# Kernel optimization log

Measured on AMD Instinct MI355X. Metric: run time of the kernel, lower is better.

The kernel has to match this reference:

```python
import jax, jax.numpy as jnp
import numpy as np
from jax import lax

CLIP = 5.0
LN_EPS = 1e-5


def _embed(feats, mean, std, W, b, g, beta):
    # InputNorm (eval mode, count>1): normalize with running stats, clamp.
    h = jnp.clip((feats - mean) / std, -CLIP, CLIP)
    h = lax.stop_gradient(h)  # torch runs InputNorm under no_grad
    # Linear + ReLU
    h = jax.nn.relu(h @ W + b)
    # LayerNorm over d_model
    mu = h.mean(-1, keepdims=True)
    var = ((h - mu) ** 2).mean(-1, keepdims=True)
    return (h - mu) / jnp.sqrt(var + LN_EPS) * g + beta


def setup_inputs() -> dict:
    key = jax.random.key(0)
    ks = jax.random.split(key, 8)
    nA, fA = 300000, 32
    nB, fB = 150000, 48
    d = 256
    B = 512
    inp = {
        "featsA": jax.random.normal(ks[0], (nA, fA), jnp.float32),
        "featsB": jax.random.normal(ks[1], (nB, fB), jnp.float32),
        "normA_mean": jnp.zeros((fA,), jnp.float32),
        "normA_std": jnp.ones((fA,), jnp.float32),
        "normB_mean": jnp.zeros((fB,), jnp.float32),
        "normB_std": jnp.ones((fB,), jnp.float32),
        "WA": jax.random.normal(ks[2], (fA, d), jnp.float32) / np.sqrt(fA),
        "bA": jnp.zeros((d,), jnp.float32),
        "lnA_g": jnp.ones((d,), jnp.float32),
        "lnA_b": jnp.zeros((d,), jnp.float32),
        "WB_": jax.random.normal(ks[3], (fB, d), jnp.float32) / np.sqrt(fB),
        "bB": jnp.zeros((d,), jnp.float32),
        "lnB_g": jnp.ones((d,), jnp.float32),
        "lnB_b": jnp.zeros((d,), jnp.float32),
        "Wback": jax.random.normal(ks[4], (d, d), jnp.float32) / np.sqrt(d),
        "bback": jnp.zeros((d,), jnp.float32),
        "Wv": jax.random.normal(ks[5], (d, 1), jnp.float32) / np.sqrt(d),
        "bv": jnp.zeros((1,), jnp.float32),
        "batch_index": jax.random.randint(ks[6], (nA + nB,), 0, B, jnp.int64)
        if jax.config.jax_enable_x64 else jax.random.randint(ks[6], (nA + nB,), 0, B, jnp.int32).astype(jnp.int32),
        "num_obs": B,
    }
    return inp


def reference(featsA, featsB, normA_mean, normA_std, normB_mean, normB_std,
              WA, bA, lnA_g, lnA_b, WB_, bB, lnB_g, lnB_b,
              Wback, bback, Wv, bv, batch_index, num_obs):
    # Per-entity-type embedding stacks, concatenated in entity-type order
    xA = _embed(featsA, normA_mean, normA_std, WA, bA, lnA_g, lnA_b)
    xB = _embed(featsB, normB_mean, normB_std, WB_, bB, lnB_g, lnB_b)
    x = jnp.concatenate([xA, xB], axis=0)          # [N, d]
    x = jax.nn.relu(x @ Wback + bback)              # backbone
    # torch_scatter mean pooling over observations
    sums = jax.ops.segment_sum(x, batch_index, num_segments=num_obs)
    counts = jax.ops.segment_sum(jnp.ones((x.shape[0],), x.dtype), batch_index,
                                 num_segments=num_obs)
    pooled = sums / jnp.maximum(counts, 1.0)[:, None]  # empty segments -> 0
    return pooled @ Wv + bv                          # [num_obs, 1]
```

## Files before the change

kernel.cpp:

```cpp
#include <hip/hip_runtime.h>

#define NSEG 512
#define NSPLIT 32

typedef __attribute__((ext_vector_type(8))) short short8;
typedef __attribute__((ext_vector_type(4))) short short4v;
typedef __attribute__((ext_vector_type(4))) float floatx4;

#define WS_WAT   0
#define WS_WBT2  16384
#define WS_W2GA  49152
#define WS_W2GB  180224
#define WS_C1A   311296
#define WS_C2A   312320
#define WS_C1B   313344
#define WS_C2B   314368
#define WS_INVA  315392
#define WS_INVB  315520
#define WS_VPART 315712
#define WS_CPART 381248
#define WS_NF    446848

__device__ __forceinline__ short f2bf(float f) {
  unsigned u = __builtin_bit_cast(unsigned, f);
  u += 0x7FFFu + ((u >> 16) & 1u);
  return (short)(u >> 16);
}

__global__ void prep_kernel(const float* __restrict__ WA, const float* __restrict__ WB,
                            const float* __restrict__ Wback,
                            const float* __restrict__ gA, const float* __restrict__ betaA,
                            const float* __restrict__ gB, const float* __restrict__ betaB,
                            const float* __restrict__ bback,
                            const float* __restrict__ sA, const float* __restrict__ sB,
                            char* __restrict__ ws) {
  short* waT  = (short*)(ws + WS_WAT);
  short* wbT2 = (short*)(ws + WS_WBT2);
  short* w2gA = (short*)(ws + WS_W2GA);
  short* w2gB = (short*)(ws + WS_W2GB);
  float* c1A = (float*)(ws + WS_C1A);
  float* c2A = (float*)(ws + WS_C2A);
  float* c1B = (float*)(ws + WS_C1B);
  float* c2B = (float*)(ws + WS_C2B);
  float* invA = (float*)(ws + WS_INVA);
  float* invB = (float*)(ws + WS_INVB);
  float* vz   = (float*)(ws + WS_VPART);
  int tid = blockIdx.x * blockDim.x + threadIdx.x;
  int stride = gridDim.x * blockDim.x;
  if (tid < 32) invA[tid] = 1.0f / sA[tid];
  if (tid < 48) invB[tid] = 1.0f / sB[tid];
  for (int i = tid; i < 32*256; i += stride) {
    int n = i >> 5, k = i & 31;
    waT[i] = f2bf(WA[k*256 + n]);
  }
  for (int i = tid; i < 256*64; i += stride) {
    int n = i >> 6, k = i & 63;
    wbT2[i] = (k < 48) ? f2bf(WB[k*256 + n]) : (short)0;
  }
  for (int i = tid; i < 256*256; i += stride) {
    int n = i >> 8, k = i & 255;
    float w = Wback[k*256 + n];
    w2gA[i] = f2bf(gA[k] * w);
    w2gB[i] = f2bf(gB[k] * w);
  }
  if (blockIdx.x < 4 && threadIdx.x < 256) {
    int n = threadIdx.x;
    int which = blockIdx.x;
    const float* coef = (which == 0) ? gA : (which == 1) ? betaA : (which == 2) ? gB : betaB;
    float a = 0.f;
    #pragma unroll 8
    for (int k = 0; k < 256; k++) a = fmaf(coef[k], Wback[k*256 + n], a);
    if (which == 0)      c1A[n] = a;
    else if (which == 1) c2A[n] = a + bback[n];
    else if (which == 2) c1B[n] = a;
    else                 c2B[n] = a + bback[n];
  }
  for (int i = tid; i < 2*NSPLIT*NSEG; i += stride) vz[i] = 0.0f;
}

__global__ __launch_bounds__(256) void norm_kernel(
    const float* __restrict__ fA, const float* __restrict__ fB,
    const float* __restrict__ mA, const float* __restrict__ mB,
    const char* __restrict__ ws, short* __restrict__ nfA, short* __restrict__ nfB,
    int rowsApad, int nA, int rowsBpad, int nB)
{
  const float* invA = (const float*)(ws + WS_INVA);
  const float* invB = (const float*)(ws + WS_INVB);
  int tid = blockIdx.x * blockDim.x + threadIdx.x;
  int stride = gridDim.x * blockDim.x;
  int chunksA = rowsApad * 4;
  int chunksB = rowsBpad * 8;
  for (int i = tid; i < chunksA + chunksB; i += stride) {
    short8 o = {0,0,0,0,0,0,0,0};
    if (i < chunksA) {
      int row = i >> 2, c0 = (i & 3) * 8;
      if (row < nA) {
        const float* fp = fA + (size_t)row*32 + c0;
        floatx4 x0 = *(const floatx4*)fp;
        floatx4 x1 = *(const floatx4*)(fp + 4);
        floatx4 mv0 = *(const floatx4*)(mA + c0);
        floatx4 mv1 = *(const floatx4*)(mA + c0 + 4);
        floatx4 iv0 = *(const floatx4*)(invA + c0);
        floatx4 iv1 = *(const floatx4*)(invA + c0 + 4);
        #pragma unroll
        for (int e = 0; e < 4; e++) {
          float h0 = fminf(fmaxf((x0[e] - mv0[e]) * iv0[e], -5.0f), 5.0f);
          float h1 = fminf(fmaxf((x1[e] - mv1[e]) * iv1[e], -5.0f), 5.0f);
          o[e] = f2bf(h0);  o[4+e] = f2bf(h1);
        }
      }
      *(short8*)(nfA + (size_t)row*32 + c0) = o;
    } else {
      int j = i - chunksA;
      int row = j >> 3, c0 = (j & 7) * 8;
      if (row < nB && c0 < 48) {
        const float* fp = fB + (size_t)row*48 + c0;
        floatx4 x0 = *(const floatx4*)fp;
        floatx4 x1 = *(const floatx4*)(fp + 4);
        floatx4 mv0 = *(const floatx4*)(mB + c0);
        floatx4 mv1 = *(const floatx4*)(mB + c0 + 4);
        floatx4 iv0 = *(const floatx4*)(invB + c0);
        floatx4 iv1 = *(const floatx4*)(invB + c0 + 4);
        #pragma unroll
        for (int e = 0; e < 4; e++) {
          float h0 = fminf(fmaxf((x0[e] - mv0[e]) * iv0[e], -5.0f), 5.0f);
          float h1 = fminf(fmaxf((x1[e] - mv1[e]) * iv1[e], -5.0f), 5.0f);
          o[e] = f2bf(h0);  o[4+e] = f2bf(h1);
        }
      }
      *(short8*)(nfB + (size_t)row*64 + c0) = o;
    }
  }
}

template <bool PRE>
__global__ __launch_bounds__(256, 4) void fused_kernel(
    const float* __restrict__ featsA, const float* __restrict__ featsB,
    const short* __restrict__ nfA, const short* __restrict__ nfB,
    const float* __restrict__ mA, const float* __restrict__ mB,
    const float* __restrict__ bA, const float* __restrict__ bB,
    const float* __restrict__ Wv, const int* __restrict__ bidx,
    const char* __restrict__ ws, float* __restrict__ vpart, float* __restrict__ cpart,
    int tilesA, int nA, int nB)
{
  __shared__ __attribute__((aligned(16))) short ztile[64*264];
  __shared__ __attribute__((aligned(16))) float sred[64][4];
  __shared__ __attribute__((aligned(16))) float s2red[64][4];
  __shared__ __attribute__((aligned(16))) float vpw[64][4];

  const int tid  = threadIdx.x;
  const int wave = tid >> 6;
  const int lane = tid & 63;
  const int l15  = lane & 15;
  const int quad = lane >> 4;

  const bool isA = (blockIdx.x < (unsigned)tilesA);
  const int  tb  = isA ? blockIdx.x : (blockIdx.x - tilesA);
  const int  r0  = tb * 64;
  const int  nrows = isA ? nA : nB;
  const int  valid = min(64, nrows - r0);
  const float* feats = isA ? featsA : featsB;
  const short* nf    = isA ? nfA : nfB;
  const float* meanp = isA ? mA : mB;
  const float* invp  = (const float*)(ws + (isA ? WS_INVA : WS_INVB));
  const float* biasp = isA ? bA : bB;
  const short* weT   = (const short*)(ws + (isA ? WS_WAT : WS_WBT2));
  const short* w2gT  = (const short*)(ws + (isA ? WS_W2GA : WS_W2GB));
  const float* c1p   = (const float*)(ws + (isA ? WS_C1A : WS_C1B));
  const float* c2p   = (const float*)(ws + (isA ? WS_C2A : WS_C2B));
  const int f       = isA ? 32 : 48;
  const int kstride = isA ? 32 : 64;
  const int ksteps  = isA ? 1 : 2;

  floatx4 acc1[4][4];
  #pragma unroll
  for (int mt = 0; mt < 4; mt++)
    #pragma unroll
    for (int nt = 0; nt < 4; nt++)
      acc1[mt][nt] = 0.0f;

  for (int kk = 0; kk < ksteps; kk++) {
    short8 bfw[4];
    #pragma unroll
    for (int nt = 0; nt < 4; nt++)
      bfw[nt] = *(const short8*)(weT + (size_t)(64*wave + 16*nt + l15) * kstride + kk*32 + quad*8);

    if (PRE) {
      #pragma unroll
      for (int mt = 0; mt < 4; mt++) {
        short8 a = *(const short8*)(nf + (size_t)(r0 + 16*mt + l15) * kstride + kk*32 + quad*8);
        #pragma unroll
        for (int nt = 0; nt < 4; nt++)
          acc1[mt][nt] = __builtin_amdgcn_mfma_f32_16x16x32_bf16(bfw[nt], a, acc1[mt][nt], 0, 0, 0);
      }
    } else {
      const int k0 = kk*32 + quad*8;
      const bool kvalid = (k0 < f);
      floatx4 mv0 = {0,0,0,0}, mv1 = {0,0,0,0}, iv0 = {1,1,1,1}, iv1 = {1,1,1,1};
      if (kvalid) {
        mv0 = *(const floatx4*)(meanp + k0);  mv1 = *(const floatx4*)(meanp + k0 + 4);
        iv0 = *(const floatx4*)(invp + k0);   iv1 = *(const floatx4*)(invp + k0 + 4);
      }
      #pragma unroll
      for (int mt = 0; mt < 4; mt++) {
        short8 a = {0,0,0,0,0,0,0,0};
        int row = 16*mt + l15;
        if (kvalid && row < valid) {
          const float* fp = feats + (size_t)(r0 + row) * f + k0;
          floatx4 x0 = *(const floatx4*)fp;
          floatx4 x1 = *(const floatx4*)(fp + 4);
          #pragma unroll
          for (int e = 0; e < 4; e++) {
            float h0 = (x0[e] - mv0[e]) * iv0[e];
            h0 = fminf(fmaxf(h0, -5.0f), 5.0f);
            a[e] = f2bf(h0);
            float h1 = (x1[e] - mv1[e]) * iv1[e];
            h1 = fminf(fmaxf(h1, -5.0f), 5.0f);
            a[4+e] = f2bf(h1);
          }
        }
        #pragma unroll
        for (int nt = 0; nt < 4; nt++)
          acc1[mt][nt] = __builtin_amdgcn_mfma_f32_16x16x32_bf16(bfw[nt], a, acc1[mt][nt], 0, 0, 0);
      }
    }
  }

  float sacc[4], s2acc[4];
  #pragma unroll
  for (int mt = 0; mt < 4; mt++) { sacc[mt] = 0.f; s2acc[mt] = 0.f; }

  #pragma unroll
  for (int nt = 0; nt < 4; nt++) {
    const int c0 = 64*wave + 16*nt + 4*quad;
    floatx4 b1v = *(const floatx4*)(biasp + c0);
    #pragma unroll
    for (int mt = 0; mt < 4; mt++) {
      short4v pk;
      #pragma unroll
      for (int r = 0; r < 4; r++) {
        float h = fmaxf(acc1[mt][nt][r] + b1v[r], 0.0f);
        sacc[mt] += h;
        s2acc[mt] = fmaf(h, h, s2acc[mt]);
        pk[r] = f2bf(h);
      }
      *(short4v*)(ztile + (16*mt + l15)*264 + c0) = pk;
    }
  }
  #pragma unroll
  for (int mt = 0; mt < 4; mt++) {
    float s = sacc[mt], s2 = s2acc[mt];
    s += __shfl_xor(s, 16, 64);  s2 += __shfl_xor(s2, 16, 64);
    s += __shfl_xor(s, 32, 64);  s2 += __shfl_xor(s2, 32, 64);
    if (lane < 16) {
      sred[16*mt + lane][wave] = s;
      s2red[16*mt + lane][wave] = s2;
    }
  }
  __syncthreads();

  float rsv[4], mrsv[4];
  #pragma unroll
  for (int mt = 0; mt < 4; mt++) {
    int row = 16*mt + l15;
    floatx4 sv  = *(const floatx4*)sred[row];
    floatx4 s2v = *(const floatx4*)s2red[row];
    float s  = sv[0] + sv[1] + sv[2] + sv[3];
    float s2 = s2v[0] + s2v[1] + s2v[2] + s2v[3];
    float mu  = s * (1.0f/256.0f);
    float var = fmaxf(s2 * (1.0f/256.0f) - mu*mu, 0.0f);
    float rs  = rsqrtf(var + 1e-5f);
    rsv[mt]  = rs;
    mrsv[mt] = mu * rs;
  }

  floatx4 acc2[4][4];
  #pragma unroll
  for (int mt = 0; mt < 4; mt++)
    #pragma unroll
    for (int nt = 0; nt < 4; nt++)
      acc2[mt][nt] = 0.0f;

  #pragma unroll 2
  for (int kk = 0; kk < 8; kk++) {
    short8 bf[4];
    #pragma unroll
    for (int nt = 0; nt < 4; nt++)
      bf[nt] = *(const short8*)(w2gT + (size_t)(64*wave + 16*nt + l15)*256 + kk*32 + quad*8);
    #pragma unroll
    for (int mt = 0; mt < 4; mt++) {
      short8 a = *(const short8*)(ztile + (16*mt + l15)*264 + kk*32 + quad*8);
      #pragma unroll
      for (int nt = 0; nt < 4; nt++)
        acc2[mt][nt] = __builtin_amdgcn_mfma_f32_16x16x32_bf16(bf[nt], a, acc2[mt][nt], 0, 0, 0);
    }
  }

  float pv[4] = {0.f, 0.f, 0.f, 0.f};
  #pragma unroll
  for (int nt = 0; nt < 4; nt++) {
    const int c0 = 64*wave + 16*nt + 4*quad;
    floatx4 c1v = *(const floatx4*)(c1p + c0);
    floatx4 c2v = *(const floatx4*)(c2p + c0);
    floatx4 wvv = *(const floatx4*)(Wv + c0);
    #pragma unroll
    for (int mt = 0; mt < 4; mt++) {
      float rs = rsv[mt], mrs = mrsv[mt];
      #pragma unroll
      for (int r = 0; r < 4; r++) {
        float t = fmaf(-mrs, c1v[r], c2v[r]);
        float y = fmaf(rs, acc2[mt][nt][r], t);
        y = fmaxf(y, 0.0f);
        pv[mt] = fmaf(y, wvv[r], pv[mt]);
      }
    }
  }
  #pragma unroll
  for (int mt = 0; mt < 4; mt++) {
    float p = pv[mt];
    p += __shfl_xor(p, 16, 64);
    p += __shfl_xor(p, 32, 64);
    if (lane < 16) vpw[16*mt + lane][wave] = p;
  }
  __syncthreads();

  if (tid < valid) {
    floatx4 vv = *(const floatx4*)vpw[tid];
    float v = vv[0] + vv[1] + vv[2] + vv[3];
    int g = (isA ? r0 : (nA + r0)) + tid;
    int seg = bidx[g];
    int split = blockIdx.x & (NSPLIT - 1);
    atomicAdd(&vpart[split*NSEG + seg], v);
    atomicAdd(&cpart[split*NSEG + seg], 1.0f);
  }
}

__global__ void final_kernel(const float* __restrict__ vpart, const float* __restrict__ cpart,
                             const float* __restrict__ bv, float* __restrict__ out, int nseg) {
  int s = blockIdx.x * blockDim.x + threadIdx.x;
  if (s < nseg) {
    float a = 0.0f, c = 0.0f;
    #pragma unroll 8
    for (int i = 0; i < NSPLIT; i++) { a += vpart[i*NSEG + s]; c += cpart[i*NSEG + s]; }
    out[s] = a / fmaxf(c, 1.0f) + bv[0];
  }
}

extern "C" void kernel_launch(void* const* d_in, const int* in_sizes, int n_in,
                              void* d_out, int out_size, void* d_ws, size_t ws_size,
                              hipStream_t stream) {
  const float* featsA = (const float*)d_in[0];
  const float* featsB = (const float*)d_in[1];
  const float* mA     = (const float*)d_in[2];
  const float* sA     = (const float*)d_in[3];
  const float* mB     = (const float*)d_in[4];
  const float* sB     = (const float*)d_in[5];
  const float* WA     = (const float*)d_in[6];
  const float* bA     = (const float*)d_in[7];
  const float* gA     = (const float*)d_in[8];
  const float* betaA  = (const float*)d_in[9];
  const float* WB     = (const float*)d_in[10];
  const float* bB     = (const float*)d_in[11];
  const float* gB     = (const float*)d_in[12];
  const float* betaB  = (const float*)d_in[13];
  const float* Wback  = (const float*)d_in[14];
  const float* bback  = (const float*)d_in[15];
  const float* Wv     = (const float*)d_in[16];
  const float* bv     = (const float*)d_in[17];
  const int*   bidx   = (const int*)d_in[18];

  const int nA = in_sizes[0] / 32;
  const int nB = in_sizes[1] / 48;
  char* ws = (char*)d_ws;
  float* vpart = (float*)(ws + WS_VPART);
  float* cpart = (float*)(ws + WS_CPART);
  float* out = (float*)d_out;

  const int tilesA = (nA + 63) / 64;
  const int tilesB = (nB + 63) / 64;
  const int rowsApad = tilesA * 64;
  const int rowsBpad = tilesB * 64;
  const size_t nfa_off = WS_NF;
  const size_t nfb_off = nfa_off + (size_t)rowsApad * 32 * 2;
  const size_t ws_need = nfb_off + (size_t)rowsBpad * 64 * 2;
  const bool pre = (ws_size >= ws_need);
  short* nfA = (short*)(ws + nfa_off);
  short* nfB = (short*)(ws + nfb_off);

  prep_kernel<<<256, 256, 0, stream>>>(WA, WB, Wback, gA, betaA, gB, betaB,
                                       bback, sA, sB, ws);

  if (pre) {
    const int chunks = rowsApad * 4 + rowsBpad * 8;
    int nblk = (chunks + 255) / 256;
    if (nblk > 2048) nblk = 2048;
    norm_kernel<<<nblk, 256, 0, stream>>>(featsA, featsB, mA, mB, ws, nfA, nfB,
                                          rowsApad, nA, rowsBpad, nB);
    fused_kernel<true><<<tilesA + tilesB, 256, 0, stream>>>(
        featsA, featsB, nfA, nfB, mA, mB, bA, bB, Wv, bidx, ws, vpart, cpart,
        tilesA, nA, nB);
  } else {
    fused_kernel<false><<<tilesA + tilesB, 256, 0, stream>>>(
        featsA, featsB, nfA, nfB, mA, mB, bA, bB, Wv, bidx, ws, vpart, cpart,
        tilesA, nA, nB);
  }

  if (out_size > 0)
    final_kernel<<<(out_size + 255) / 256, 256, 0, stream>>>(vpart, cpart, bv, out, out_size);
}
```

Measured before the change: 309.0 us.

## Fuse weight prep into normalization kernel and specialize tile body per entity type

Merges the weight-preparation kernel and the feature normalization kernel into one launch, with each block computing the inverse std into shared memory so normalization need not wait for a prior kernel. Adds a templated per-type tile body with compile-time K stride and step count, plus hoisted base pointers for the MFMA loops. The aim is to cut one launch and its serialization gap and to let the compiler unroll and simplify address math in the main fused kernel. When workspace is too small, the fused kernel still reads invA/invB from the workspace, which the merged kernel writes, so that fallback path keeps working.

```diff
diff --git a/kernel.cpp b/kernel.cpp
--- a/kernel.cpp
+++ b/kernel.cpp
@@ -27,67 +27,67 @@
   return (short)(u >> 16);
 }
 
-__global__ void prep_kernel(const float* __restrict__ WA, const float* __restrict__ WB,
-                            const float* __restrict__ Wback,
-                            const float* __restrict__ gA, const float* __restrict__ betaA,
-                            const float* __restrict__ gB, const float* __restrict__ betaB,
-                            const float* __restrict__ bback,
-                            const float* __restrict__ sA, const float* __restrict__ sB,
-                            char* __restrict__ ws) {
-  short* waT  = (short*)(ws + WS_WAT);
-  short* wbT2 = (short*)(ws + WS_WBT2);
-  short* w2gA = (short*)(ws + WS_W2GA);
-  short* w2gB = (short*)(ws + WS_W2GB);
-  float* c1A = (float*)(ws + WS_C1A);
-  float* c2A = (float*)(ws + WS_C2A);
-  float* c1B = (float*)(ws + WS_C1B);
-  float* c2B = (float*)(ws + WS_C2B);
-  float* invA = (float*)(ws + WS_INVA);
-  float* invB = (float*)(ws + WS_INVB);
-  float* vz   = (float*)(ws + WS_VPART);
+__global__ __launch_bounds__(256) void prep_norm_kernel(
+    const float* __restrict__ fA, const float* __restrict__ fB,
+    const float* __restrict__ mA, const float* __restrict__ mB,
+    const float* __restrict__ sA, const float* __restrict__ sB,
+    const float* __restrict__ WA, const float* __restrict__ WB,
+    const float* __restrict__ Wback,
+    const float* __restrict__ gA, const float* __restrict__ betaA,
+    const float* __restrict__ gB, const float* __restrict__ betaB,
+    const float* __restrict__ bback,
+    char* __restrict__ ws, short* __restrict__ nfA, short* __restrict__ nfB,
+    int rowsApad, int nA, int rowsBpad, int nB)
+{
+  __shared__ float sinv[80];
+  if (threadIdx.x < 32) sinv[threadIdx.x] = 1.0f / sA[threadIdx.x];
+  else if (threadIdx.x < 80) sinv[threadIdx.x] = 1.0f / sB[threadIdx.x - 32];
+  __syncthreads();
+  const float* invAl = sinv;
+  const float* invBl = sinv + 32;
+
   int tid = blockIdx.x * blockDim.x + threadIdx.x;
   int stride = gridDim.x * blockDim.x;
-  if (tid < 32) invA[tid] = 1.0f / sA[tid];
-  if (tid < 48) invB[tid] = 1.0f / sB[tid];
-  for (int i = tid; i < 32*256; i += stride) {
-    int n = i >> 5, k = i & 31;
-    waT[i] = f2bf(WA[k*256 + n]);
-  }
-  for (int i = tid; i < 256*64; i += stride) {
-    int n = i >> 6, k = i & 63;
-    wbT2[i] = (k < 48) ? f2bf(WB[k*256 + n]) : (short)0;
-  }
-  for (int i = tid; i < 256*256; i += stride) {
-    int n = i >> 8, k = i & 255;
-    float w = Wback[k*256 + n];
-    w2gA[i] = f2bf(gA[k] * w);
-    w2gB[i] = f2bf(gB[k] * w);
-  }
-  if (blockIdx.x < 4 && threadIdx.x < 256) {
+
+  if (blockIdx.x < 4) {
     int n = threadIdx.x;
     int which = blockIdx.x;
     const float* coef = (which == 0) ? gA : (which == 1) ? betaA : (which == 2) ? gB : betaB;
     float a = 0.f;
     #pragma unroll 8
     for (int k = 0; k < 256; k++) a = fmaf(coef[k], Wback[k*256 + n], a);
-    if (which == 0)      c1A[n] = a;
-    else if (which == 1) c2A[n] = a + bback[n];
-    else if (which == 2) c1B[n] = a;
-    else                 c2B[n] = a + bback[n];
-  }
-  for (int i = tid; i < 2*NSPLIT*NSEG; i += stride) vz[i] = 0.0f;
-}
-
-__global__ __launch_bounds__(256) void norm_kernel(
-    const float* __restrict__ fA, const float* __restrict__ fB,
-    const float* __restrict__ mA, const float* __restrict__ mB,
-    const char* __restrict__ ws, short* __restrict__ nfA, short* __restrict__ nfB,
-    int rowsApad, int nA, int rowsBpad, int nB)
-{
-  const float* invA = (const float*)(ws + WS_INVA);
-  const float* invB = (const float*)(ws + WS_INVB);
-  int tid = blockIdx.x * blockDim.x + threadIdx.x;
-  int stride = gridDim.x * blockDim.x;
+    float* dst = (float*)(ws + ((which == 0) ? WS_C1A : (which == 1) ? WS_C2A
+                               : (which == 2) ? WS_C1B : WS_C2B));
+    dst[n] = a + ((which & 1) ? bback[n] : 0.0f);
+  }
+
+  {
+    short* waT  = (short*)(ws + WS_WAT);
+    short* wbT2 = (short*)(ws + WS_WBT2);
+    short* w2gA = (short*)(ws + WS_W2GA);
+    short* w2gB = (short*)(ws + WS_W2GB);
+    float* invA = (float*)(ws + WS_INVA);
+    float* invB = (float*)(ws + WS_INVB);
+    float* vz   = (float*)(ws + WS_VPART);
+    if (tid < 32) invA[tid] = invAl[tid];
+    if (tid < 48) invB[tid] = invBl[tid];
+    for (int i = tid; i < 32*256; i += stride) {
+      int n = i >> 5, k = i & 31;
+      waT[i] = f2bf(WA[k*256 + n]);
+    }
+    for (int i = tid; i < 256*64; i += stride) {
+      int n = i >> 6, k = i & 63;
+      wbT2[i] = (k < 48) ? f2bf(WB[k*256 + n]) : (short)0;
+    }
+    for (int i = tid; i < 256*256; i += stride) {
+      int n = i >> 8, k = i & 255;
+      float w = Wback[k*256 + n];
+      w2gA[i] = f2bf(gA[k] * w);
+      w2gB[i] = f2bf(gB[k] * w);
+    }
+    for (int i = tid; i < 2*NSPLIT*NSEG; i += stride) vz[i] = 0.0f;
+  }
+
   int chunksA = rowsApad * 4;
   int chunksB = rowsBpad * 8;
   for (int i = tid; i < chunksA + chunksB; i += stride) {
@@ -100,8 +100,8 @@
         floatx4 x1 = *(const floatx4*)(fp + 4);
         floatx4 mv0 = *(const floatx4*)(mA + c0);
         floatx4 mv1 = *(const floatx4*)(mA + c0 + 4);
-        floatx4 iv0 = *(const floatx4*)(invA + c0);
-        floatx4 iv1 = *(const floatx4*)(invA + c0 + 4);
+        floatx4 iv0 = *(const floatx4*)(invAl + c0);
+        floatx4 iv1 = *(const floatx4*)(invAl + c0 + 4);
         #pragma unroll
         for (int e = 0; e < 4; e++) {
           float h0 = fminf(fmaxf((x0[e] - mv0[e]) * iv0[e], -5.0f), 5.0f);
@@ -119,8 +119,8 @@
         floatx4 x1 = *(const floatx4*)(fp + 4);
         floatx4 mv0 = *(const floatx4*)(mB + c0);
         floatx4 mv1 = *(const floatx4*)(mB + c0 + 4);
-        floatx4 iv0 = *(const floatx4*)(invB + c0);
-        floatx4 iv1 = *(const floatx4*)(invB + c0 + 4);
+        floatx4 iv0 = *(const floatx4*)(invBl + c0);
+        floatx4 iv1 = *(const floatx4*)(invBl + c0 + 4);
         #pragma unroll
         for (int e = 0; e < 4; e++) {
           float h0 = fminf(fmaxf((x0[e] - mv0[e]) * iv0[e], -5.0f), 5.0f);
@@ -130,6 +130,158 @@
       }
       *(short8*)(nfB + (size_t)row*64 + c0) = o;
     }
+  }
+}
+
+template <int KSTR, int KSTEPS>
+__device__ __forceinline__ void tile_body(
+    const short* __restrict__ nfb,
+    const short* __restrict__ weT, const short* __restrict__ w2gT,
+    const float* __restrict__ biasp, const float* __restrict__ c1p,
+    const float* __restrict__ c2p, const float* __restrict__ Wv,
+    const int* __restrict__ bidx, float* __restrict__ vpart, float* __restrict__ cpart,
+    short* ztile, float (*sred)[4], float (*s2red)[4], float (*vpw)[4],
+    int valid, int gbase, int split, int tid)
+{
+  const int wave = tid >> 6;
+  const int lane = tid & 63;
+  const int l15  = lane & 15;
+  const int quad = lane >> 4;
+
+  floatx4 acc1[4][4];
+  #pragma unroll
+  for (int mt = 0; mt < 4; mt++)
+    #pragma unroll
+    for (int nt = 0; nt < 4; nt++)
+      acc1[mt][nt] = 0.0f;
+
+  const short* nfp = nfb + l15*KSTR + quad*8;
+  const short* wep = weT + (64*wave + l15)*KSTR + quad*8;
+  #pragma unroll
+  for (int kk = 0; kk < KSTEPS; kk++) {
+    short8 bfw[4];
+    #pragma unroll
+    for (int nt = 0; nt < 4; nt++)
+      bfw[nt] = *(const short8*)(wep + nt*16*KSTR + kk*32);
+    #pragma unroll
+    for (int mt = 0; mt < 4; mt++) {
+      short8 a = *(const short8*)(nfp + mt*16*KSTR + kk*32);
+      #pragma unroll
+      for (int nt = 0; nt < 4; nt++)
+        acc1[mt][nt] = __builtin_amdgcn_mfma_f32_16x16x32_bf16(bfw[nt], a, acc1[mt][nt], 0, 0, 0);
+    }
+  }
+
+  float sacc[4] = {0.f,0.f,0.f,0.f}, s2acc[4] = {0.f,0.f,0.f,0.f};
+  {
+    short* ztw = ztile + l15*264 + 64*wave + 4*quad;
+    const float* bp = biasp + 64*wave + 4*quad;
+    #pragma unroll
+    for (int nt = 0; nt < 4; nt++) {
+      floatx4 b1v = *(const floatx4*)(bp + 16*nt);
+      #pragma unroll
+      for (int mt = 0; mt < 4; mt++) {
+        short4v pk;
+        #pragma unroll
+        for (int r = 0; r < 4; r++) {
+          float h = fmaxf(acc1[mt][nt][r] + b1v[r], 0.0f);
+          sacc[mt] += h;
+          s2acc[mt] = fmaf(h, h, s2acc[mt]);
+          pk[r] = f2bf(h);
+        }
+        *(short4v*)(ztw + mt*16*264 + nt*16) = pk;
+      }
+    }
+  }
+  #pragma unroll
+  for (int mt = 0; mt < 4; mt++) {
+    float s = sacc[mt], s2 = s2acc[mt];
+    s += __shfl_xor(s, 16, 64);  s2 += __shfl_xor(s2, 16, 64);
+    s += __shfl_xor(s, 32, 64);  s2 += __shfl_xor(s2, 32, 64);
+    if (lane < 16) {
+      sred[16*mt + lane][wave] = s;
+      s2red[16*mt + lane][wave] = s2;
+    }
+  }
+  __syncthreads();
+
+  floatx4 acc2[4][4];
+  #pragma unroll
+  for (int mt = 0; mt < 4; mt++)
+    #pragma unroll
+    for (int nt = 0; nt < 4; nt++)
+      acc2[mt][nt] = 0.0f;
+
+  const short* wgp = w2gT + (64*wave + l15)*256 + quad*8;
+  const short* ztp = ztile + l15*264 + quad*8;
+  #pragma unroll 2
+  for (int kk = 0; kk < 8; kk++) {
+    short8 bf[4];
+    #pragma unroll
+    for (int nt = 0; nt < 4; nt++)
+      bf[nt] = *(const short8*)(wgp + nt*16*256 + kk*32);
+    #pragma unroll
+    for (int mt = 0; mt < 4; mt++) {
+      short8 a = *(const short8*)(ztp + mt*16*264 + kk*32);
+      #pragma unroll
+      for (int nt = 0; nt < 4; nt++)
+        acc2[mt][nt] = __builtin_amdgcn_mfma_f32_16x16x32_bf16(bf[nt], a, acc2[mt][nt], 0, 0, 0);
+    }
+  }
+
+  float rsv[4], mrsv[4];
+  #pragma unroll
+  for (int mt = 0; mt < 4; mt++) {
+    int row = 16*mt + l15;
+    floatx4 sv  = *(const floatx4*)sred[row];
+    floatx4 s2v = *(const floatx4*)s2red[row];
+    float s  = sv[0] + sv[1] + sv[2] + sv[3];
+    float s2 = s2v[0] + s2v[1] + s2v[2] + s2v[3];
+    float mu  = s * (1.0f/256.0f);
+    float var = fmaxf(s2 * (1.0f/256.0f) - mu*mu, 0.0f);
+    float rs  = rsqrtf(var + 1e-5f);
+    rsv[mt]  = rs;
+    mrsv[mt] = mu * rs;
+  }
+
+  float pv[4] = {0.f, 0.f, 0.f, 0.f};
+  {
+    const float* c1b = c1p + 64*wave + 4*quad;
+    const float* c2b = c2p + 64*wave + 4*quad;
+    const float* wvb = Wv  + 64*wave + 4*quad;
+    #pragma unroll
+    for (int nt = 0; nt < 4; nt++) {
+      floatx4 c1v = *(const floatx4*)(c1b + 16*nt);
+      floatx4 c2v = *(const floatx4*)(c2b + 16*nt);
+      floatx4 wvv = *(const floatx4*)(wvb + 16*nt);
+      #pragma unroll
+      for (int mt = 0; mt < 4; mt++) {
+        float rs = rsv[mt], mrs = mrsv[mt];
+        #pragma unroll
+        for (int r = 0; r < 4; r++) {
+          float t = fmaf(-mrs, c1v[r], c2v[r]);
+          float y = fmaf(rs, acc2[mt][nt][r], t);
+          y = fmaxf(y, 0.0f);
+          pv[mt] = fmaf(y, wvv[r], pv[mt]);
+        }
+      }
+    }
+  }
+  #pragma unroll
+  for (int mt = 0; mt < 4; mt++) {
+    float p = pv[mt];
+    p += __shfl_xor(p, 16, 64);
+    p += __shfl_xor(p, 32, 64);
+    if (lane < 16) vpw[16*mt + lane][wave] = p;
+  }
+  __syncthreads();
+
+  if (tid < valid) {
+    floatx4 vv = *(const floatx4*)vpw[tid];
+    float v = vv[0] + vv[1] + vv[2] + vv[3];
+    int seg = bidx[gbase + tid];
+    atomicAdd(&vpart[split*NSEG + seg], v);
+    atomicAdd(&cpart[split*NSEG + seg], 1.0f);
   }
 }
 
@@ -149,25 +301,38 @@
   __shared__ __attribute__((aligned(16))) float vpw[64][4];
 
   const int tid  = threadIdx.x;
-  const int wave = tid >> 6;
-  const int lane = tid & 63;
-  const int l15  = lane & 15;
-  const int quad = lane >> 4;
-
   const bool isA = (blockIdx.x < (unsigned)tilesA);
   const int  tb  = isA ? blockIdx.x : (blockIdx.x - tilesA);
   const int  r0  = tb * 64;
   const int  nrows = isA ? nA : nB;
   const int  valid = min(64, nrows - r0);
-  const float* feats = isA ? featsA : featsB;
-  const short* nf    = isA ? nfA : nfB;
-  const float* meanp = isA ? mA : mB;
-  const float* invp  = (const float*)(ws + (isA ? WS_INVA : WS_INVB));
+  const int  gbase = (isA ? r0 : (nA + r0));
+  const int  split = blockIdx.x & (NSPLIT - 1);
   const float* biasp = isA ? bA : bB;
   const short* weT   = (const short*)(ws + (isA ? WS_WAT : WS_WBT2));
   const short* w2gT  = (const short*)(ws + (isA ? WS_W2GA : WS_W2GB));
   const float* c1p   = (const float*)(ws + (isA ? WS_C1A : WS_C1B));
   const float* c2p   = (const float*)(ws + (isA ? WS_C2A : WS_C2B));
+
+  if (PRE) {
+    if (isA)
+      tile_body<32,1>(nfA + (size_t)r0*32, weT, w2gT, biasp, c1p, c2p, Wv,
+                      bidx, vpart, cpart, ztile, sred, s2red, vpw,
+                      valid, gbase, split, tid);
+    else
+      tile_body<64,2>(nfB + (size_t)r0*64, weT, w2gT, biasp, c1p, c2p, Wv,
+                      bidx, vpart, cpart, ztile, sred, s2red, vpw,
+                      valid, gbase, split, tid);
+    return;
+  }
+
+  const int wave = tid >> 6;
+  const int lane = tid & 63;
+  const int l15  = lane & 15;
+  const int quad = lane >> 4;
+  const float* feats = isA ? featsA : featsB;
+  const float* meanp = isA ? mA : mB;
+  const float* invp  = (const float*)(ws + (isA ? WS_INVA : WS_INVB));
   const int f       = isA ? 32 : 48;
   const int kstride = isA ? 32 : 64;
   const int ksteps  = isA ? 1 : 2;
@@ -184,52 +349,38 @@
     #pragma unroll
     for (int nt = 0; nt < 4; nt++)
       bfw[nt] = *(const short8*)(weT + (size_t)(64*wave + 16*nt + l15) * kstride + kk*32 + quad*8);
-
-    if (PRE) {
-      #pragma unroll
-      for (int mt = 0; mt < 4; mt++) {
-        short8 a = *(const short8*)(nf + (size_t)(r0 + 16*mt + l15) * kstride + kk*32 + quad*8);
+    const int k0 = kk*32 + quad*8;
+    const bool kvalid = (k0 < f);
+    floatx4 mv0 = {0,0,0,0}, mv1 = {0,0,0,0}, iv0 = {1,1,1,1}, iv1 = {1,1,1,1};
+    if (kvalid) {
+      mv0 = *(const floatx4*)(meanp + k0);  mv1 = *(const floatx4*)(meanp + k0 + 4);
+      iv0 = *(const floatx4*)(invp + k0);   iv1 = *(const floatx4*)(invp + k0 + 4);
+    }
+    #pragma unroll
+    for (int mt = 0; mt < 4; mt++) {
+      short8 a = {0,0,0,0,0,0,0,0};
+      int row = 16*mt + l15;
+      if (kvalid && row < valid) {
+        const float* fp = feats + (size_t)(r0 + row) * f + k0;
+        floatx4 x0 = *(const floatx4*)fp;
+        floatx4 x1 = *(const floatx4*)(fp + 4);
         #pragma unroll
-        for (int nt = 0; nt < 4; nt++)
-          acc1[mt][nt] = __builtin_amdgcn_mfma_f32_16x16x32_bf16(bfw[nt], a, acc1[mt][nt], 0, 0, 0);
-      }
-    } else {
-      const int k0 = kk*32 + quad*8;
-      const bool kvalid = (k0 < f);
-      floatx4 mv0 = {0,0,0,0}, mv1 = {0,0,0,0}, iv0 = {1,1,1,1}, iv1 = {1,1,1,1};
-      if (kvalid) {
-        mv0 = *(const floatx4*)(meanp + k0);  mv1 = *(const floatx4*)(meanp + k0 + 4);
-        iv0 = *(const floatx4*)(invp + k0);   iv1 = *(const floatx4*)(invp + k0 + 4);
-      }
-      #pragma unroll
-      for (int mt = 0; mt < 4; mt++) {
-        short8 a = {0,0,0,0,0,0,0,0};
-        int row = 16*mt + l15;
-        if (kvalid && row < valid) {
-          const float* fp = feats + (size_t)(r0 + row) * f + k0;
-          floatx4 x0 = *(const floatx4*)fp;
-          floatx4 x1 = *(const floatx4*)(fp + 4);
-          #pragma unroll
-          for (int e = 0; e < 4; e++) {
-            float h0 = (x0[e] - mv0[e]) * iv0[e];
-            h0 = fminf(fmaxf(h0, -5.0f), 5.0f);
-            a[e] = f2bf(h0);
-            float h1 = (x1[e] - mv1[e]) * iv1[e];
-            h1 = fminf(fmaxf(h1, -5.0f), 5.0f);
-            a[4+e] = f2bf(h1);
-          }
+        for (int e = 0; e < 4; e++) {
+          float h0 = (x0[e] - mv0[e]) * iv0[e];
+          h0 = fminf(fmaxf(h0, -5.0f), 5.0f);
+          a[e] = f2bf(h0);
+          float h1 = (x1[e] - mv1[e]) * iv1[e];
+          h1 = fminf(fmaxf(h1, -5.0f), 5.0f);
+          a[4+e] = f2bf(h1);
         }
-        #pragma unroll
-        for (int nt = 0; nt < 4; nt++)
-          acc1[mt][nt] = __builtin_amdgcn_mfma_f32_16x16x32_bf16(bfw[nt], a, acc1[mt][nt], 0, 0, 0);
-      }
-    }
-  }
-
-  float sacc[4], s2acc[4];
-  #pragma unroll
-  for (int mt = 0; mt < 4; mt++) { sacc[mt] = 0.f; s2acc[mt] = 0.f; }
-
+      }
+      #pragma unroll
+      for (int nt = 0; nt < 4; nt++)
+        acc1[mt][nt] = __builtin_amdgcn_mfma_f32_16x16x32_bf16(bfw[nt], a, acc1[mt][nt], 0, 0, 0);
+    }
+  }
+
+  float sacc[4] = {0.f,0.f,0.f,0.f}, s2acc[4] = {0.f,0.f,0.f,0.f};
   #pragma unroll
   for (int nt = 0; nt < 4; nt++) {
     const int c0 = 64*wave + 16*nt + 4*quad;
@@ -258,6 +409,27 @@
     }
   }
   __syncthreads();
+
+  floatx4 acc2[4][4];
+  #pragma unroll
+  for (int mt = 0; mt < 4; mt++)
+    #pragma unroll
+    for (int nt = 0; nt < 4; nt++)
+      acc2[mt][nt] = 0.0f;
+  #pragma unroll 2
+  for (int kk = 0; kk < 8; kk++) {
+    short8 bf[4];
+    #pragma unroll
+    for (int nt = 0; nt < 4; nt++)
+      bf[nt] = *(const short8*)(w2gT + (size_t)(64*wave + 16*nt + l15)*256 + kk*32 + quad*8);
+    #pragma unroll
+    for (int mt = 0; mt < 4; mt++) {
+      short8 a = *(const short8*)(ztile + (16*mt + l15)*264 + kk*32 + quad*8);
+      #pragma unroll
+      for (int nt = 0; nt < 4; nt++)
+        acc2[mt][nt] = __builtin_amdgcn_mfma_f32_16x16x32_bf16(bf[nt], a, acc2[mt][nt], 0, 0, 0);
+    }
+  }
 
   float rsv[4], mrsv[4];
   #pragma unroll
@@ -274,28 +446,6 @@
     mrsv[mt] = mu * rs;
   }
 
-  floatx4 acc2[4][4];
-  #pragma unroll
-  for (int mt = 0; mt < 4; mt++)
-    #pragma unroll
-    for (int nt = 0; nt < 4; nt++)
-      acc2[mt][nt] = 0.0f;
-
-  #pragma unroll 2
-  for (int kk = 0; kk < 8; kk++) {
-    short8 bf[4];
-    #pragma unroll
-    for (int nt = 0; nt < 4; nt++)
-      bf[nt] = *(const short8*)(w2gT + (size_t)(64*wave + 16*nt + l15)*256 + kk*32 + quad*8);
-    #pragma unroll
-    for (int mt = 0; mt < 4; mt++) {
-      short8 a = *(const short8*)(ztile + (16*mt + l15)*264 + kk*32 + quad*8);
-      #pragma unroll
-      for (int nt = 0; nt < 4; nt++)
-        acc2[mt][nt] = __builtin_amdgcn_mfma_f32_16x16x32_bf16(bf[nt], a, acc2[mt][nt], 0, 0, 0);
-    }
-  }
-
   float pv[4] = {0.f, 0.f, 0.f, 0.f};
   #pragma unroll
   for (int nt = 0; nt < 4; nt++) {
@@ -327,9 +477,7 @@
   if (tid < valid) {
     floatx4 vv = *(const floatx4*)vpw[tid];
     float v = vv[0] + vv[1] + vv[2] + vv[3];
-    int g = (isA ? r0 : (nA + r0)) + tid;
-    int seg = bidx[g];
-    int split = blockIdx.x & (NSPLIT - 1);
+    int seg = bidx[gbase + tid];
     atomicAdd(&vpart[split*NSEG + seg], v);
     atomicAdd(&cpart[split*NSEG + seg], 1.0f);
   }
@@ -387,15 +535,14 @@
   short* nfA = (short*)(ws + nfa_off);
   short* nfB = (short*)(ws + nfb_off);
 
-  prep_kernel<<<256, 256, 0, stream>>>(WA, WB, Wback, gA, betaA, gB, betaB,
-                                       bback, sA, sB, ws);
+  const int chunks = rowsApad * 4 + rowsBpad * 8;
+  int nblk = (chunks + 255) / 256;
+  if (nblk > 2048) nblk = 2048;
+  prep_norm_kernel<<<nblk, 256, 0, stream>>>(
+      featsA, featsB, mA, mB, sA, sB, WA, WB, Wback, gA, betaA, gB, betaB,
+      bback, ws, nfA, nfB, rowsApad, nA, rowsBpad, nB);
 
   if (pre) {
-    const int chunks = rowsApad * 4 + rowsBpad * 8;
-    int nblk = (chunks + 255) / 256;
-    if (nblk > 2048) nblk = 2048;
-    norm_kernel<<<nblk, 256, 0, stream>>>(featsA, featsB, mA, mB, ws, nfA, nfB,
-                                          rowsApad, nA, rowsBpad, nB);
     fused_kernel<true><<<tilesA + tilesB, 256, 0, stream>>>(
         featsA, featsB, nfA, nfB, mA, mB, bA, bB, Wv, bidx, ws, vpart, cpart,
         tilesA, nA, nB);
```

Result: slower. 315.2 us (+2.0%).
